# Kernel tuning notes

Hardware: AMD Instinct MI355X
Metric: run time of the kernel (lower is better)

The kernel has to match this reference:

```python
import jax, jax.numpy as jnp
import numpy as np

N_NODES = 20000
N_EDGES = 320000
D_IN = 32 * 32 * 3  # 3072


def gcn_layer(x, W, b, src, dst):
    # Lign GCN(nn.Linear): dense transform, then sum-aggregation over edges
    h = x @ W + b                                            # [N, d_out]
    msg = jax.ops.segment_sum(h[src], dst, num_segments=N_NODES)  # neighbor sum
    return h + msg                                           # self + neighbors


def setup_inputs() -> dict:
    key = jax.random.key(0)
    ks = jax.random.split(key, 12)
    def w(k, shape, fan_in):
        return jax.random.normal(k, shape, jnp.float32) * (1.0 / np.sqrt(fan_in))
    return {
        "features": jax.random.normal(ks[0], (N_NODES, D_IN), jnp.float32),
        "src": jax.random.randint(ks[1], (N_EDGES,), 0, N_NODES),
        "dst": jax.random.randint(ks[2], (N_EDGES,), 0, N_NODES),
        "W1": w(ks[3], (D_IN, 1000), D_IN), "b1": jnp.zeros((1000,), jnp.float32),
        "W2": w(ks[4], (1000, 300), 1000), "b2": jnp.zeros((300,), jnp.float32),
        "W3": w(ks[5], (300, 20), 300),    "b3": jnp.zeros((20,), jnp.float32),
        "W4": w(ks[6], (20, 10), 20),      "b4": jnp.zeros((10,), jnp.float32),
    }


def reference(features, src, dst, W1, b1, W2, b2, W3, b3, W4, b4):
    x = features.reshape(-1, D_IN)
    x = jax.nn.relu(gcn_layer(x, W1, b1, src, dst))
    x = jax.nn.relu(gcn_layer(x, W2, b2, src, dst))
    x = gcn_layer(x, W3, b3, src, dst)
    return jnp.tanh(gcn_layer(x, W4, b4, src, dst))
```

## Files before the change

kernel.cpp:

```cpp
#include <hip/hip_runtime.h>
#include <math.h>

#define N_NODES 20000
#define N_EDGES 320000
#define D_IN    3072

#define M_PAD   20096
#define N1_PAD  1024
#define LDH1    1024
#define K2_PAD  1024
#define N2_PAD  384
#define LDH2    384

typedef short bf16x8 __attribute__((ext_vector_type(8)));
typedef float f32x4  __attribute__((ext_vector_type(4)));
typedef int   i32x4  __attribute__((ext_vector_type(4)));

#define GLOAD_LDS16(g, l) __builtin_amdgcn_global_load_lds( \
    (const __attribute__((address_space(1))) void*)(g),     \
    (__attribute__((address_space(3))) void*)(l), 16, 0, 0)

__device__ inline unsigned short f2bf(float x) {
    union { float f; unsigned u; } v; v.f = x;
    unsigned r = (v.u + 0x7FFFu + ((v.u >> 16) & 1u)) >> 16;
    return (unsigned short)r;
}
__device__ inline float bf2f(unsigned short h) {
    union { float f; unsigned u; } v; v.u = ((unsigned)h) << 16;
    return v.f;
}


__global__ void zero_counts_kernel(int* __restrict__ counts) {
    int i = blockIdx.x * blockDim.x + threadIdx.x;
    if (i < N_NODES) counts[i] = 0;
}

__global__ void count_kernel(const int* __restrict__ dst, int* __restrict__ counts) {
    int e = blockIdx.x * blockDim.x + threadIdx.x;
    if (e < N_EDGES) atomicAdd(&counts[dst[e]], 1);
}

__global__ void scan_kernel(const int* __restrict__ counts, int* __restrict__ row_start,
                            int* __restrict__ cursor) {
    __shared__ int part[1024];
    const int T = 1024;
    int t = threadIdx.x;
    const int chunk = (N_NODES + T - 1) / T;
    int lo = t * chunk;
    int hi = lo + chunk; if (hi > N_NODES) hi = N_NODES;
    int s = 0;
    for (int i = lo; i < hi; ++i) s += counts[i];
    part[t] = s;
    __syncthreads();
    for (int off = 1; off < T; off <<= 1) {
        int v = (t >= off) ? part[t - off] : 0;
        __syncthreads();
        part[t] += v;
        __syncthreads();
    }
    int run = part[t] - s;
    for (int i = lo; i < hi; ++i) {
        row_start[i] = run;
        cursor[i] = run;
        run += counts[i];
    }
    if (t == T - 1) row_start[N_NODES] = run;
}

__global__ void scatter_kernel(const int* __restrict__ src, const int* __restrict__ dst,
                               int* __restrict__ cursor, int* __restrict__ esrc) {
    int e = blockIdx.x * blockDim.x + threadIdx.x;
    if (e < N_EDGES) {
        int pos = atomicAdd(&cursor[dst[e]], 1);
        esrc[pos] = src[e];
    }
}


__global__ __launch_bounds__(256)
void convA_i8_kernel(const float* __restrict__ X, signed char* __restrict__ Aq1,
                     signed char* __restrict__ Aq2, float* __restrict__ sA) {
    __shared__ float red[256];
    const int row = blockIdx.x;
    const int t = threadIdx.x;
    const float* xr = X + (size_t)row * D_IN;
    float v[12];
    float mx = 0.f;
    #pragma unroll
    for (int c = 0; c < 3; ++c) {
        float4 f = *reinterpret_cast<const float4*>(&xr[(t + c * 256) * 4]);
        v[c*4+0] = f.x; v[c*4+1] = f.y; v[c*4+2] = f.z; v[c*4+3] = f.w;
        mx = fmaxf(mx, fmaxf(fmaxf(fabsf(f.x), fabsf(f.y)), fmaxf(fabsf(f.z), fabsf(f.w))));
    }
    red[t] = mx;
    __syncthreads();
    for (int off = 128; off > 0; off >>= 1) {
        if (t < off) red[t] = fmaxf(red[t], red[t + off]);
        __syncthreads();
    }
    const float rmax = red[0];
    const float s   = (rmax > 0.f) ? rmax / 16256.f : 1.f;
    const float inv = 16256.f / ((rmax > 0.f) ? rmax : 1.f);
    if (t == 0) sA[row] = s;
    #pragma unroll
    for (int c = 0; c < 3; ++c) {
        signed char q1v[4], q2v[4];
        #pragma unroll
        for (int e = 0; e < 4; ++e) {
            int q = __float2int_rn(v[c*4+e] * inv);
            q = min(max(q, -16256), 16256);
            int q1 = (q + 64) >> 7;
            int q2 = q - (q1 << 7);
            q1v[e] = (signed char)q1; q2v[e] = (signed char)q2;
        }
        size_t base = (size_t)row * D_IN + (size_t)(t + c * 256) * 4;
        *reinterpret_cast<char4*>(&Aq1[base]) = make_char4(q1v[0], q1v[1], q1v[2], q1v[3]);
        *reinterpret_cast<char4*>(&Aq2[base]) = make_char4(q2v[0], q2v[1], q2v[2], q2v[3]);
    }
}


__global__ __launch_bounds__(256)
void zero_swbits_kernel(unsigned* __restrict__ bits, int NPAD) {
    int n = blockIdx.x * blockDim.x + threadIdx.x;
    if (n < NPAD) bits[n] = 0u;
}

__global__ __launch_bounds__(256)
void colmaxW_kernel(const float* __restrict__ W, unsigned* __restrict__ bits,
                    int K, int N, int KCHUNK) {
    int n = blockIdx.x * blockDim.x + threadIdx.x;
    if (n >= N) return;
    int k0 = blockIdx.y * KCHUNK;
    int k1 = min(k0 + KCHUNK, K);
    float mx = 0.f;
    for (int k = k0; k < k1; ++k)
        mx = fmaxf(mx, fabsf(W[(size_t)k * N + n]));
    atomicMax(&bits[n], __float_as_uint(mx));
}

__global__ __launch_bounds__(256)
void finalize_sw_kernel(unsigned* __restrict__ bits, float* __restrict__ sW, int NPAD) {
    int n = blockIdx.x * blockDim.x + threadIdx.x;
    if (n >= NPAD) return;
    float mx = __uint_as_float(bits[n]);
    sW[n] = (mx > 0.f) ? mx / 16256.f : 1.f;
}

__global__ __launch_bounds__(256)
void convW_i8_kernel(const float* __restrict__ W, const float* __restrict__ sW,
                     signed char* __restrict__ Wq1T, signed char* __restrict__ Wq2T,
                     int K, int N, int K_PAD) {
    __shared__ float sh[32][33];
    const int t  = threadIdx.x;
    const int tx = t & 31;
    const int ty = t >> 5;
    const int n0 = blockIdx.x * 32;
    const int k0 = blockIdx.y * 32;
    #pragma unroll
    for (int it = 0; it < 4; ++it) {
        int k = k0 + ty + it * 8;
        int n = n0 + tx;
        sh[ty + it * 8][tx] = (k < K && n < N) ? W[(size_t)k * N + n] : 0.f;
    }
    __syncthreads();
    #pragma unroll
    for (int it = 0; it < 4; ++it) {
        int n = n0 + ty + it * 8;
        int k = k0 + tx;
        float v = sh[tx][ty + it * 8];
        float s = sW[n];
        int q = __float2int_rn(v / s);
        q = min(max(q, -16256), 16256);
        int q1 = (q + 64) >> 7;
        int q2 = q - (q1 << 7);
        Wq1T[(size_t)n * K_PAD + k] = (signed char)q1;
        Wq2T[(size_t)n * K_PAD + k] = (signed char)q2;
    }
}


#define GBM 128
#define GBN 128

#define ISSUE2I(p0, p1, ss) do { \
    GLOAD_LDS16(p0, &lds[ss][wid * 1024]); \
    GLOAD_LDS16(p1, &lds[ss][wid * 1024 + 4096]); \
    p0 += 64; p1 += 64; } while (0)

__global__ __launch_bounds__(256, 2)
void gemm_i8_mfma_kernel(const signed char* __restrict__ Aq1,
                         const signed char* __restrict__ Aq2,
                         const signed char* __restrict__ Bq1T,
                         const signed char* __restrict__ Bq2T,
                         const float* __restrict__ sA, const float* __restrict__ sB,
                         const float* __restrict__ bias, float* __restrict__ H,
                         int K, int NB, int ldh, int nbias) {
    __shared__ __align__(16) char lds[4][8192];

    const int t    = threadIdx.x;
    const int wid  = t >> 6;
    const int lane = t & 63;
    const int wr   = wid >> 1;
    const int wc   = wid & 1;

    const int orig = blockIdx.x;
    const int nwg  = gridDim.x;
    const int xcd  = orig & 7, loc = orig >> 3;
    const int q    = nwg >> 3, r = nwg & 7;
    const int wgid = (xcd < r ? xcd * (q + 1) : r * (q + 1) + (xcd - r) * q) + loc;
    const int m0   = (wgid / NB) * GBM;
    const int n0   = (wgid % NB) * GBN;

    i32x4 accH[4][4] = {};
    i32x4 accM[4][4] = {};

    const int byt0 = wid * 1024 + lane * 16;
    const int byt1 = byt0 + 4096;
    const int r0 = byt0 >> 6, r1 = byt1 >> 6;
    const int cs0 = (byt0 & 63) ^ (((r0 >> 1) & 3) << 4);
    const int cs1 = (byt1 & 63) ^ (((r1 >> 1) & 3) << 4);

    const signed char* pA10 = Aq1  + (size_t)(m0 + r0) * K + cs0;
    const signed char* pA11 = Aq1  + (size_t)(m0 + r1) * K + cs1;
    const signed char* pA20 = Aq2  + (size_t)(m0 + r0) * K + cs0;
    const signed char* pA21 = Aq2  + (size_t)(m0 + r1) * K + cs1;
    const signed char* pB10 = Bq1T + (size_t)(n0 + r0) * K + cs0;
    const signed char* pB11 = Bq1T + (size_t)(n0 + r1) * K + cs1;
    const signed char* pB20 = Bq2T + (size_t)(n0 + r0) * K + cs0;
    const signed char* pB21 = Bq2T + (size_t)(n0 + r1) * K + cs1;

    const int fr   = lane & 15;
    const int kbs  = ((lane >> 4) << 4) ^ (((fr >> 1) & 3) << 4);
    const int arow = wr * 64;
    const int brow = wc * 64;

    ISSUE2I(pA10, pA11, 0);
    ISSUE2I(pB10, pB11, 2);
    ISSUE2I(pB20, pB21, 3);
    ISSUE2I(pA20, pA21, 1);

    const int NT = K >> 6;
    i32x4 a1[4], b1[4], b2[4], a2[4];

    for (int tt = 0; tt < NT; ++tt) {
        if (tt == 0) asm volatile("s_waitcnt vmcnt(4)" ::: "memory");
        else         asm volatile("s_waitcnt vmcnt(2)" ::: "memory");
        __builtin_amdgcn_s_barrier();
        #pragma unroll
        for (int i = 0; i < 4; ++i)
            a1[i] = *(const i32x4*)(&lds[0][(arow + i * 16 + fr) * 64 + kbs]);
        #pragma unroll
        for (int j = 0; j < 4; ++j)
            b1[j] = *(const i32x4*)(&lds[2][(brow + j * 16 + fr) * 64 + kbs]);
        if (tt > 0) ISSUE2I(pA20, pA21, 1);
        __builtin_amdgcn_s_setprio(1);
        #pragma unroll
        for (int i = 0; i < 4; ++i)
            #pragma unroll
            for (int j = 0; j < 4; ++j)
                accH[i][j] = __builtin_amdgcn_mfma_i32_16x16x64_i8(a1[i], b1[j], accH[i][j], 0, 0, 0);
        __builtin_amdgcn_s_setprio(0);
        asm volatile("s_waitcnt vmcnt(2)" ::: "memory");
        __builtin_amdgcn_s_barrier();
        #pragma unroll
        for (int j = 0; j < 4; ++j)
            b2[j] = *(const i32x4*)(&lds[3][(brow + j * 16 + fr) * 64 + kbs]);
        if (tt < NT - 1) {
            ISSUE2I(pA10, pA11, 0);
            ISSUE2I(pB10, pB11, 2);
        }
        __builtin_amdgcn_s_setprio(1);
        #pragma unroll
        for (int i = 0; i < 4; ++i)
            #pragma unroll
            for (int j = 0; j < 4; ++j)
                accM[i][j] = __builtin_amdgcn_mfma_i32_16x16x64_i8(a1[i], b2[j], accM[i][j], 0, 0, 0);
        __builtin_amdgcn_s_setprio(0);
        if (tt < NT - 1) asm volatile("s_waitcnt vmcnt(4)" ::: "memory");
        else             asm volatile("s_waitcnt vmcnt(0)" ::: "memory");
        __builtin_amdgcn_s_barrier();
        #pragma unroll
        for (int i = 0; i < 4; ++i)
            a2[i] = *(const i32x4*)(&lds[1][(arow + i * 16 + fr) * 64 + kbs]);
        if (tt < NT - 1) ISSUE2I(pB20, pB21, 3);
        __builtin_amdgcn_s_setprio(1);
        #pragma unroll
        for (int i = 0; i < 4; ++i)
            #pragma unroll
            for (int j = 0; j < 4; ++j)
                accM[i][j] = __builtin_amdgcn_mfma_i32_16x16x64_i8(a2[i], b1[j], accM[i][j], 0, 0, 0);
        __builtin_amdgcn_s_setprio(0);
    }

    #pragma unroll
    for (int i = 0; i < 4; ++i) {
        #pragma unroll
        for (int j = 0; j < 4; ++j) {
            int row = m0 + wr * 64 + i * 16 + (lane >> 4) * 4;
            int col = n0 + wc * 64 + j * 16 + (lane & 15);
            float bv = (col < nbias) ? bias[col] : 0.f;
            float sw = sB[col];
            #pragma unroll
            for (int r2 = 0; r2 < 4; ++r2) {
                float sa = sA[row + r2];
                float v = sa * sw * (16384.f * (float)accH[i][j][r2] + 128.f * (float)accM[i][j][r2]) + bv;
                H[(size_t)(row + r2) * ldh + col] = v;
            }
        }
    }
}


__global__ __launch_bounds__(256)
void convW_kernel(const float* __restrict__ W, unsigned short* __restrict__ WhiT,
                  unsigned short* __restrict__ WloT, int K, int N, int K_PAD) {
    __shared__ float sh[32][33];
    const int t  = threadIdx.x;
    const int tx = t & 31;
    const int ty = t >> 5;
    const int n0 = blockIdx.x * 32;
    const int k0 = blockIdx.y * 32;
    #pragma unroll
    for (int it = 0; it < 4; ++it) {
        int k = k0 + ty + it * 8;
        int n = n0 + tx;
        sh[ty + it * 8][tx] = (k < K && n < N) ? W[(size_t)k * N + n] : 0.f;
    }
    __syncthreads();
    #pragma unroll
    for (int it = 0; it < 4; ++it) {
        int n = n0 + ty + it * 8;
        int k = k0 + tx;
        float v = sh[tx][ty + it * 8];
        unsigned short h = f2bf(v);
        unsigned short l = f2bf(v - bf2f(h));
        WhiT[(size_t)n * K_PAD + k] = h;
        WloT[(size_t)n * K_PAD + k] = l;
    }
}


#define GBK 32

#define ISSUE2(p0, p1, ss) do { \
    GLOAD_LDS16(p0, &lds[ss][wid * 1024]); \
    GLOAD_LDS16(p1, &lds[ss][wid * 1024 + 4096]); \
    p0 += GBK; p1 += GBK; } while (0)

__global__ __launch_bounds__(256, 3)
void gemm_split_mfma_kernel(const unsigned short* __restrict__ Ahi,
                            const unsigned short* __restrict__ Alo,
                            const unsigned short* __restrict__ BhiT,
                            const unsigned short* __restrict__ BloT,
                            const float* __restrict__ bias, float* __restrict__ H,
                            int K, int NB, int ldh, int nbias) {
    __shared__ __align__(16) char lds[4][8192];

    const int t    = threadIdx.x;
    const int wid  = t >> 6;
    const int lane = t & 63;
    const int wr   = wid >> 1;
    const int wc   = wid & 1;

    const int orig = blockIdx.x;
    const int nwg  = gridDim.x;
    const int xcd  = orig & 7, loc = orig >> 3;
    const int q    = nwg >> 3, r = nwg & 7;
    const int wgid = (xcd < r ? xcd * (q + 1) : r * (q + 1) + (xcd - r) * q) + loc;
    const int m0   = (wgid / NB) * GBM;
    const int n0   = (wgid % NB) * GBN;

    f32x4 acc[4][4] = {};

    const int byt0 = wid * 1024 + lane * 16;
    const int byt1 = byt0 + 4096;
    const int r0 = byt0 >> 6, r1 = byt1 >> 6;
    const int cs0 = (byt0 & 63) ^ (((r0 >> 1) & 3) << 4);
    const int cs1 = (byt1 & 63) ^ (((r1 >> 1) & 3) << 4);

    const unsigned short* pAh0 = Ahi  + (size_t)(m0 + r0) * K + (cs0 >> 1);
    const unsigned short* pAh1 = Ahi  + (size_t)(m0 + r1) * K + (cs1 >> 1);
    const unsigned short* pAl0 = Alo  + (size_t)(m0 + r0) * K + (cs0 >> 1);
    const unsigned short* pAl1 = Alo  + (size_t)(m0 + r1) * K + (cs1 >> 1);
    const unsigned short* pBh0 = BhiT + (size_t)(n0 + r0) * K + (cs0 >> 1);
    const unsigned short* pBh1 = BhiT + (size_t)(n0 + r1) * K + (cs1 >> 1);
    const unsigned short* pBl0 = BloT + (size_t)(n0 + r0) * K + (cs0 >> 1);
    const unsigned short* pBl1 = BloT + (size_t)(n0 + r1) * K + (cs1 >> 1);

    const int fr   = lane & 15;
    const int kbs  = ((lane >> 4) << 4) ^ (((fr >> 1) & 3) << 4);
    const int arow = wr * 64;
    const int brow = wc * 64;

    ISSUE2(pAh0, pAh1, 0);
    ISSUE2(pBh0, pBh1, 2);
    ISSUE2(pBl0, pBl1, 3);
    ISSUE2(pAl0, pAl1, 1);

    const int NT = K >> 5;
    bf16x8 ahi[4], bhi[4], blo[4], alo[4];

    for (int tt = 0; tt < NT; ++tt) {
        if (tt == 0) asm volatile("s_waitcnt vmcnt(4)" ::: "memory");
        else         asm volatile("s_waitcnt vmcnt(2)" ::: "memory");
        __builtin_amdgcn_s_barrier();
        #pragma unroll
        for (int i = 0; i < 4; ++i)
            ahi[i] = *(const bf16x8*)(&lds[0][(arow + i * 16 + fr) * 64 + kbs]);
        #pragma unroll
        for (int j = 0; j < 4; ++j)
            bhi[j] = *(const bf16x8*)(&lds[2][(brow + j * 16 + fr) * 64 + kbs]);
        if (tt > 0) ISSUE2(pAl0, pAl1, 1);
        __builtin_amdgcn_s_setprio(1);
        #pragma unroll
        for (int i = 0; i < 4; ++i)
            #pragma unroll
            for (int j = 0; j < 4; ++j)
                acc[i][j] = __builtin_amdgcn_mfma_f32_16x16x32_bf16(ahi[i], bhi[j], acc[i][j], 0, 0, 0);
        __builtin_amdgcn_s_setprio(0);
        asm volatile("s_waitcnt vmcnt(2)" ::: "memory");
        __builtin_amdgcn_s_barrier();
        #pragma unroll
        for (int j = 0; j < 4; ++j)
            blo[j] = *(const bf16x8*)(&lds[3][(brow + j * 16 + fr) * 64 + kbs]);
        if (tt < NT - 1) {
            ISSUE2(pAh0, pAh1, 0);
            ISSUE2(pBh0, pBh1, 2);
        }
        __builtin_amdgcn_s_setprio(1);
        #pragma unroll
        for (int i = 0; i < 4; ++i)
            #pragma unroll
            for (int j = 0; j < 4; ++j)
                acc[i][j] = __builtin_amdgcn_mfma_f32_16x16x32_bf16(ahi[i], blo[j], acc[i][j], 0, 0, 0);
        __builtin_amdgcn_s_setprio(0);
        if (tt < NT - 1) asm volatile("s_waitcnt vmcnt(4)" ::: "memory");
        else             asm volatile("s_waitcnt vmcnt(0)" ::: "memory");
        __builtin_amdgcn_s_barrier();
        #pragma unroll
        for (int i = 0; i < 4; ++i)
            alo[i] = *(const bf16x8*)(&lds[1][(arow + i * 16 + fr) * 64 + kbs]);
        if (tt < NT - 1) ISSUE2(pBl0, pBl1, 3);
        __builtin_amdgcn_s_setprio(1);
        #pragma unroll
        for (int i = 0; i < 4; ++i)
            #pragma unroll
            for (int j = 0; j < 4; ++j)
                acc[i][j] = __builtin_amdgcn_mfma_f32_16x16x32_bf16(alo[i], bhi[j], acc[i][j], 0, 0, 0);
        __builtin_amdgcn_s_setprio(0);
    }

    #pragma unroll
    for (int i = 0; i < 4; ++i) {
        #pragma unroll
        for (int j = 0; j < 4; ++j) {
            int row = m0 + wr * 64 + i * 16 + (lane >> 4) * 4;
            int col = n0 + wc * 64 + j * 16 + (lane & 15);
            float bv = (col < nbias) ? bias[col] : 0.f;
            #pragma unroll
            for (int r2 = 0; r2 < 4; ++r2)
                H[(size_t)(row + r2) * ldh + col] = acc[i][j][r2] + bv;
        }
    }
}


#define BM 64
#define BN 64
#define BKT 16
#define TM 4
#define TN 4

__global__ __launch_bounds__(256)
void gemm_bias_kernel(const float* __restrict__ X, const float* __restrict__ W,
                      const float* __restrict__ bias, float* __restrict__ H,
                      int M, int N, int K) {
    __shared__ float As[BKT][BM];
    __shared__ float Bs[BKT][BN];

    const int t  = threadIdx.x;
    const int tx = t & 15;
    const int ty = t >> 4;
    const int m0 = blockIdx.y * BM;
    const int n0 = blockIdx.x * BN;

    float acc[TM][TN] = {};

    const int arow = t >> 2;
    const int ak0  = (t & 3) * 4;
    const int brow = t >> 4;
    const int bn0  = (t & 15) * 4;

    for (int k0 = 0; k0 < K; k0 += BKT) {
        {
            float4 v = make_float4(0.f, 0.f, 0.f, 0.f);
            int gm = m0 + arow;
            int gk = k0 + ak0;
            if (gm < M) {
                if (gk + 3 < K) {
                    v = *reinterpret_cast<const float4*>(&X[(long)gm * K + gk]);
                } else {
                    float tmp[4] = {0.f, 0.f, 0.f, 0.f};
                    for (int i = 0; i < 4; ++i)
                        if (gk + i < K) tmp[i] = X[(long)gm * K + gk + i];
                    v = make_float4(tmp[0], tmp[1], tmp[2], tmp[3]);
                }
            }
            As[ak0 + 0][arow] = v.x;
            As[ak0 + 1][arow] = v.y;
            As[ak0 + 2][arow] = v.z;
            As[ak0 + 3][arow] = v.w;
        }
        {
            float4 v = make_float4(0.f, 0.f, 0.f, 0.f);
            int gk = k0 + brow;
            int gn = n0 + bn0;
            if (gk < K) {
                if (gn + 3 < N) {
                    v = *reinterpret_cast<const float4*>(&W[(long)gk * N + gn]);
                } else {
                    float tmp[4] = {0.f, 0.f, 0.f, 0.f};
                    for (int i = 0; i < 4; ++i)
                        if (gn + i < N) tmp[i] = W[(long)gk * N + gn + i];
                    v = make_float4(tmp[0], tmp[1], tmp[2], tmp[3]);
                }
            }
            *reinterpret_cast<float4*>(&Bs[brow][bn0]) = v;
        }
        __syncthreads();

        #pragma unroll
        for (int kk = 0; kk < BKT; ++kk) {
            float a[TM], b[TN];
            *reinterpret_cast<float4*>(a) = *reinterpret_cast<const float4*>(&As[kk][ty * TM]);
            *reinterpret_cast<float4*>(b) = *reinterpret_cast<const float4*>(&Bs[kk][tx * TN]);
            #pragma unroll
            for (int i = 0; i < TM; ++i)
                #pragma unroll
                for (int j = 0; j < TN; ++j)
                    acc[i][j] += a[i] * b[j];
        }
        __syncthreads();
    }

    #pragma unroll
    for (int i = 0; i < TM; ++i) {
        int gm = m0 + ty * TM + i;
        if (gm >= M) continue;
        #pragma unroll
        for (int j = 0; j < TN; ++j) {
            int gn = n0 + tx * TN + j;
            if (gn < N) H[(long)gm * N + gn] = acc[i][j] + bias[gn];
        }
    }
}


__global__ __launch_bounds__(256)
void aggregate_bf16_kernel(const float* __restrict__ H, const int* __restrict__ row_start,
                           const int* __restrict__ esrc, unsigned short* __restrict__ Xhi,
                           unsigned short* __restrict__ Xlo, int d, int ld_in, int kpad) {
    const int node = blockIdx.x;
    const int f = threadIdx.x * 4;
    if (f >= kpad) return;
    if (f >= d) {
        ushort4 z = make_ushort4(0, 0, 0, 0);
        *reinterpret_cast<ushort4*>(&Xhi[(size_t)node * kpad + f]) = z;
        *reinterpret_cast<ushort4*>(&Xlo[(size_t)node * kpad + f]) = z;
        return;
    }
    const int beg = row_start[node];
    const int end = row_start[node + 1];
    float4 acc = *reinterpret_cast<const float4*>(&H[(size_t)node * ld_in + f]);
    for (int i = beg; i < end; ++i) {
        float4 v = *reinterpret_cast<const float4*>(&H[(size_t)esrc[i] * ld_in + f]);
        acc.x += v.x; acc.y += v.y; acc.z += v.z; acc.w += v.w;
    }
    acc.x = fmaxf(acc.x, 0.f); acc.y = fmaxf(acc.y, 0.f);
    acc.z = fmaxf(acc.z, 0.f); acc.w = fmaxf(acc.w, 0.f);
    unsigned short h0 = f2bf(acc.x), h1 = f2bf(acc.y), h2 = f2bf(acc.z), h3 = f2bf(acc.w);
    unsigned short l0 = f2bf(acc.x - bf2f(h0));
    unsigned short l1 = f2bf(acc.y - bf2f(h1));
    unsigned short l2 = f2bf(acc.z - bf2f(h2));
    unsigned short l3 = f2bf(acc.w - bf2f(h3));
    *reinterpret_cast<ushort4*>(&Xhi[(size_t)node * kpad + f]) = make_ushort4(h0, h1, h2, h3);
    *reinterpret_cast<ushort4*>(&Xlo[(size_t)node * kpad + f]) = make_ushort4(l0, l1, l2, l3);
}

__global__ __launch_bounds__(128)
void agg2_gemm3_kernel(const float* __restrict__ H2, const int* __restrict__ row_start,
                       const int* __restrict__ esrc, const float* __restrict__ W3,
                       const float* __restrict__ b3, float* __restrict__ h3) {
    __shared__ float x3s[304];
    __shared__ float part[6][20];
    const int node = blockIdx.x;
    const int t = threadIdx.x;
    const int beg = row_start[node];
    const int end = row_start[node + 1];
    if (t < 75) {
        const int f = t * 4;
        float4 acc = *reinterpret_cast<const float4*>(&H2[(size_t)node * LDH2 + f]);
        for (int i = beg; i < end; ++i) {
            float4 v = *reinterpret_cast<const float4*>(&H2[(size_t)esrc[i] * LDH2 + f]);
            acc.x += v.x; acc.y += v.y; acc.z += v.z; acc.w += v.w;
        }
        x3s[f + 0] = fmaxf(acc.x, 0.f);
        x3s[f + 1] = fmaxf(acc.y, 0.f);
        x3s[f + 2] = fmaxf(acc.z, 0.f);
        x3s[f + 3] = fmaxf(acc.w, 0.f);
    }
    __syncthreads();
    if (t < 120) {
        const int j = t % 20, g = t / 20;
        float s = 0.f;
        #pragma unroll 5
        for (int k = g * 50; k < g * 50 + 50; ++k)
            s += x3s[k] * W3[k * 20 + j];
        part[g][j] = s;
    }
    __syncthreads();
    if (t < 20) {
        float s = b3[t];
        #pragma unroll
        for (int g = 0; g < 6; ++g) s += part[g][t];
        h3[(size_t)node * 20 + t] = s;
    }
}

__global__ __launch_bounds__(64)
void agg3_gemm4_kernel(const float* __restrict__ h3, const int* __restrict__ row_start,
                       const int* __restrict__ esrc, const float* __restrict__ W4,
                       const float* __restrict__ b4, float* __restrict__ h4) {
    __shared__ float x4s[20];
    const int node = blockIdx.x;
    const int t = threadIdx.x;
    const int beg = row_start[node];
    const int end = row_start[node + 1];
    if (t < 20) {
        float acc = h3[(size_t)node * 20 + t];
        for (int i = beg; i < end; ++i)
            acc += h3[(size_t)esrc[i] * 20 + t];
        x4s[t] = acc;
    }
    __syncthreads();
    if (t < 10) {
        float s = b4[t];
        #pragma unroll
        for (int k = 0; k < 20; ++k) s += x4s[k] * W4[k * 10 + t];
        h4[(size_t)node * 10 + t] = s;
    }
}

template <int ACT>
__global__ __launch_bounds__(64)
void aggregate_small_kernel(const float* __restrict__ H, const int* __restrict__ row_start,
                            const int* __restrict__ esrc, float* __restrict__ out,
                            int d, int ld_in, int ld_out) {
    const int node = blockIdx.x;
    const int f = threadIdx.x;
    if (f >= d) return;
    const int beg = row_start[node];
    const int end = row_start[node + 1];
    float acc = H[(size_t)node * ld_in + f];
    for (int i = beg; i < end; ++i)
        acc += H[(size_t)esrc[i] * ld_in + f];
    if (ACT == 1) acc = fmaxf(acc, 0.f);
    if (ACT == 2) acc = tanhf(acc);
    out[(size_t)node * ld_out + f] = acc;
}

template <int ACT>
__global__ __launch_bounds__(256)
void aggregate_kernel(const float* __restrict__ H, const int* __restrict__ row_start,
                      const int* __restrict__ esrc, float* __restrict__ out,
                      int d, int ld_in) {
    const int node = blockIdx.x;
    const int t = threadIdx.x;
    const int beg = row_start[node];
    const int end = row_start[node + 1];
    float acc[4] = {0.f, 0.f, 0.f, 0.f};
    #pragma unroll
    for (int j = 0; j < 4; ++j) {
        int f = t + j * 256;
        if (f < d) acc[j] = H[(size_t)node * ld_in + f];
    }
    for (int i = beg; i < end; ++i) {
        const size_t b = (size_t)esrc[i] * ld_in;
        #pragma unroll
        for (int j = 0; j < 4; ++j) {
            int f = t + j * 256;
            if (f < d) acc[j] += H[b + f];
        }
    }
    #pragma unroll
    for (int j = 0; j < 4; ++j) {
        int f = t + j * 256;
        if (f < d) {
            float v = acc[j];
            if (ACT == 1) v = fmaxf(v, 0.f);
            if (ACT == 2) v = tanhf(v);
            out[(size_t)node * d + f] = v;
        }
    }
}


extern "C" void kernel_launch(void* const* d_in, const int* in_sizes, int n_in,
                              void* d_out, int out_size, void* d_ws, size_t ws_size,
                              hipStream_t stream) {
    const float* features = (const float*)d_in[0];
    const int*   src      = (const int*)d_in[1];
    const int*   dst      = (const int*)d_in[2];
    const float* W1 = (const float*)d_in[3];  const float* b1 = (const float*)d_in[4];
    const float* W2 = (const float*)d_in[5];  const float* b2 = (const float*)d_in[6];
    const float* W3 = (const float*)d_in[7];  const float* b3 = (const float*)d_in[8];
    const float* W4 = (const float*)d_in[9];  const float* b4 = (const float*)d_in[10];
    float* out = (float*)d_out;
    char* ws = (char*)d_ws;

    const size_t SZ_AQ   = (size_t)M_PAD * D_IN;
    const size_t OFF_AQ1 = 0;
    const size_t OFF_AQ2 = SZ_AQ;
    const size_t OFF_H1  = 2 * SZ_AQ;
    const size_t SZ_H1   = (size_t)M_PAD * LDH1 * 4;
    const size_t OFF_W1Q1 = OFF_H1 + SZ_H1;
    const size_t SZ_W1Q  = (size_t)N1_PAD * D_IN;
    const size_t OFF_W1Q2 = OFF_W1Q1 + SZ_W1Q;
    const size_t OFF_SA  = OFF_W1Q2 + SZ_W1Q;
    const size_t OFF_SW1 = OFF_SA + (size_t)M_PAD * 4;
    const size_t OFF_W2T = OFF_SW1 + (size_t)N1_PAD * 4;
    const size_t SZ_W2T  = (size_t)N2_PAD * K2_PAD * 2;
    const size_t OFF_CSR = OFF_W2T + 2 * SZ_W2T;
    const size_t SZ_CSR  = (size_t)(N_NODES * 3 + 1 + N_EDGES) * 4;
    const size_t WS_NEED = OFF_CSR + SZ_CSR;

    const size_t OFF_X2H = 0;
    const size_t OFF_X2L = (size_t)M_PAD * K2_PAD * 2;
    const size_t OFF_H2  = 2 * OFF_X2L;
    const size_t OFF_H3  = OFF_H1;
    const size_t OFF_H4  = OFF_H1 + 1600000;

    const bool use_mfma = (ws_size >= WS_NEED);
    size_t csr_off = use_mfma ? OFF_CSR : (size_t)2 * N_NODES * 1000 * 4;
    int* counts    = (int*)(ws + csr_off);
    int* row_start = counts + N_NODES;
    int* cursor    = row_start + N_NODES + 1;
    int* esrc      = cursor + N_NODES;

    zero_counts_kernel<<<(N_NODES + 255) / 256, 256, 0, stream>>>(counts);
    count_kernel<<<(N_EDGES + 255) / 256, 256, 0, stream>>>(dst, counts);
    scan_kernel<<<1, 1024, 0, stream>>>(counts, row_start, cursor);
    scatter_kernel<<<(N_EDGES + 255) / 256, 256, 0, stream>>>(src, dst, cursor, esrc);

    if (use_mfma) {
        signed char*    Aq1   = (signed char*)(ws + OFF_AQ1);
        signed char*    Aq2   = (signed char*)(ws + OFF_AQ2);
        float*          H1    = (float*)(ws + OFF_H1);
        signed char*    W1q1T = (signed char*)(ws + OFF_W1Q1);
        signed char*    W1q2T = (signed char*)(ws + OFF_W1Q2);
        float*          sA    = (float*)(ws + OFF_SA);
        float*          sW1   = (float*)(ws + OFF_SW1);
        unsigned*       sW1b  = (unsigned*)(ws + OFF_SW1);
        unsigned short* W2hiT = (unsigned short*)(ws + OFF_W2T);
        unsigned short* W2loT = (unsigned short*)(ws + OFF_W2T + SZ_W2T);
        unsigned short* X2hi  = (unsigned short*)(ws + OFF_X2H);
        unsigned short* X2lo  = (unsigned short*)(ws + OFF_X2L);
        float*          H2    = (float*)(ws + OFF_H2);
        float*          h3    = (float*)(ws + OFF_H3);
        float*          h4    = (float*)(ws + OFF_H4);

        convA_i8_kernel<<<N_NODES, 256, 0, stream>>>(features, Aq1, Aq2, sA);
        zero_swbits_kernel<<<N1_PAD / 256, 256, 0, stream>>>(sW1b, N1_PAD);
        colmaxW_kernel<<<dim3((1000 + 255) / 256, 24), 256, 0, stream>>>(W1, sW1b, D_IN, 1000, 128);
        finalize_sw_kernel<<<N1_PAD / 256, 256, 0, stream>>>(sW1b, sW1, N1_PAD);
        convW_i8_kernel<<<dim3(N1_PAD / 32, D_IN / 32), 256, 0, stream>>>(
            W1, sW1, W1q1T, W1q2T, D_IN, 1000, D_IN);
        gemm_i8_mfma_kernel<<<(N1_PAD / GBN) * (M_PAD / GBM), 256, 0, stream>>>(
            Aq1, Aq2, W1q1T, W1q2T, sA, sW1, b1, H1, D_IN, N1_PAD / GBN, LDH1, 1000);
        aggregate_bf16_kernel<<<N_NODES, 256, 0, stream>>>(
            H1, row_start, esrc, X2hi, X2lo, 1000, LDH1, K2_PAD);

        convW_kernel<<<dim3(N2_PAD / 32, K2_PAD / 32), 256, 0, stream>>>(W2, W2hiT, W2loT, 1000, 300, K2_PAD);
        gemm_split_mfma_kernel<<<(N2_PAD / GBN) * (M_PAD / GBM), 256, 0, stream>>>(
            X2hi, X2lo, W2hiT, W2loT, b2, H2, K2_PAD, N2_PAD / GBN, LDH2, 300);

        agg2_gemm3_kernel<<<N_NODES, 128, 0, stream>>>(H2, row_start, esrc, W3, b3, h3);
        agg3_gemm4_kernel<<<N_NODES, 64, 0, stream>>>(h3, row_start, esrc, W4, b4, h4);
        aggregate_small_kernel<2><<<N_NODES, 64, 0, stream>>>(h4, row_start, esrc, out, 10, 10, 10);
    } else {
        const size_t BUF = (size_t)N_NODES * 1000 * 4;
        float* bufA = (float*)ws;
        float* bufB = (float*)(ws + BUF);

        dim3 g1((1000 + BN - 1) / BN, (N_NODES + BM - 1) / BM);
        gemm_bias_kernel<<<g1, 256, 0, stream>>>(features, W1, b1, bufA, N_NODES, 1000, D_IN);
        aggregate_kernel<1><<<N_NODES, 256, 0, stream>>>(bufA, row_start, esrc, bufB, 1000, 1000);

        dim3 g2((300 + BN - 1) / BN, (N_NODES + BM - 1) / BM);
        gemm_bias_kernel<<<g2, 256, 0, stream>>>(bufB, W2, b2, bufA, N_NODES, 300, 1000);
        aggregate_kernel<1><<<N_NODES, 256, 0, stream>>>(bufA, row_start, esrc, bufB, 300, 300);

        dim3 g3((20 + BN - 1) / BN, (N_NODES + BM - 1) / BM);
        gemm_bias_kernel<<<g3, 256, 0, stream>>>(bufB, W3, b3, bufA, N_NODES, 20, 300);
        aggregate_kernel<0><<<N_NODES, 256, 0, stream>>>(bufA, row_start, esrc, bufB, 20, 20);

        dim3 g4((10 + BN - 1) / BN, (N_NODES + BM - 1) / BM);
        gemm_bias_kernel<<<g4, 256, 0, stream>>>(bufB, W4, b4, bufA, N_NODES, 10, 20);
        aggregate_kernel<2><<<N_NODES, 256, 0, stream>>>(bufA, row_start, esrc, out, 10, 10);
    }
}
```

Baseline: 727.4 us.

## Store layer-1 output as bf16 and run layer-2 GEMM with split int8 MFMA

The layer-1 GEMM is templated so it can write its output as bf16 instead of fp32, which halves the bytes the first aggregation gathers. The aggregation now quantizes each aggregated node row into two int8 parts with a per-row scale. The layer-2 GEMM reuses the split int8 MFMA kernel in place of the bf16 hi/lo split kernel, with W2 quantized the same way. Launch bounds are raised to 3 waves per SIMD. The risks are lower precision from storing H1 as bf16 and from per-row int8 quantization, a block-wide max reduction added to the aggregation, and possible register pressure at the higher occupancy.

Result: slower. 1.418 ms (+95.0%).

```diff
diff --git a/kernel.cpp b/kernel.cpp
--- a/kernel.cpp
+++ b/kernel.cpp
@@ -189,13 +189,14 @@
     GLOAD_LDS16(p1, &lds[ss][wid * 1024 + 4096]); \
     p0 += 64; p1 += 64; } while (0)
 
-__global__ __launch_bounds__(256, 2)
+template <int OUTBF>
+__global__ __launch_bounds__(256, 3)
 void gemm_i8_mfma_kernel(const signed char* __restrict__ Aq1,
                          const signed char* __restrict__ Aq2,
                          const signed char* __restrict__ Bq1T,
                          const signed char* __restrict__ Bq2T,
                          const float* __restrict__ sA, const float* __restrict__ sB,
-                         const float* __restrict__ bias, float* __restrict__ H,
+                         const float* __restrict__ bias, void* __restrict__ Hout,
                          int K, int NB, int ldh, int nbias) {
     __shared__ __align__(16) char lds[4][8192];
 
@@ -306,162 +307,9 @@
             for (int r2 = 0; r2 < 4; ++r2) {
                 float sa = sA[row + r2];
                 float v = sa * sw * (16384.f * (float)accH[i][j][r2] + 128.f * (float)accM[i][j][r2]) + bv;
-                H[(size_t)(row + r2) * ldh + col] = v;
+                if (OUTBF) ((unsigned short*)Hout)[(size_t)(row + r2) * ldh + col] = f2bf(v);
+                else       ((float*)Hout)[(size_t)(row + r2) * ldh + col] = v;
             }
-        }
-    }
-}
-
-
-__global__ __launch_bounds__(256)
-void convW_kernel(const float* __restrict__ W, unsigned short* __restrict__ WhiT,
-                  unsigned short* __restrict__ WloT, int K, int N, int K_PAD) {
-    __shared__ float sh[32][33];
-    const int t  = threadIdx.x;
-    const int tx = t & 31;
-    const int ty = t >> 5;
-    const int n0 = blockIdx.x * 32;
-    const int k0 = blockIdx.y * 32;
-    #pragma unroll
-    for (int it = 0; it < 4; ++it) {
-        int k = k0 + ty + it * 8;
-        int n = n0 + tx;
-        sh[ty + it * 8][tx] = (k < K && n < N) ? W[(size_t)k * N + n] : 0.f;
-    }
-    __syncthreads();
-    #pragma unroll
-    for (int it = 0; it < 4; ++it) {
-        int n = n0 + ty + it * 8;
-        int k = k0 + tx;
-        float v = sh[tx][ty + it * 8];
-        unsigned short h = f2bf(v);
-        unsigned short l = f2bf(v - bf2f(h));
-        WhiT[(size_t)n * K_PAD + k] = h;
-        WloT[(size_t)n * K_PAD + k] = l;
-    }
-}
-
-
-#define GBK 32
-
-#define ISSUE2(p0, p1, ss) do { \
-    GLOAD_LDS16(p0, &lds[ss][wid * 1024]); \
-    GLOAD_LDS16(p1, &lds[ss][wid * 1024 + 4096]); \
-    p0 += GBK; p1 += GBK; } while (0)
-
-__global__ __launch_bounds__(256, 3)
-void gemm_split_mfma_kernel(const unsigned short* __restrict__ Ahi,
-                            const unsigned short* __restrict__ Alo,
-                            const unsigned short* __restrict__ BhiT,
-                            const unsigned short* __restrict__ BloT,
-                            const float* __restrict__ bias, float* __restrict__ H,
-                            int K, int NB, int ldh, int nbias) {
-    __shared__ __align__(16) char lds[4][8192];
-
-    const int t    = threadIdx.x;
-    const int wid  = t >> 6;
-    const int lane = t & 63;
-    const int wr   = wid >> 1;
-    const int wc   = wid & 1;
-
-    const int orig = blockIdx.x;
-    const int nwg  = gridDim.x;
-    const int xcd  = orig & 7, loc = orig >> 3;
-    const int q    = nwg >> 3, r = nwg & 7;
-    const int wgid = (xcd < r ? xcd * (q + 1) : r * (q + 1) + (xcd - r) * q) + loc;
-    const int m0   = (wgid / NB) * GBM;
-    const int n0   = (wgid % NB) * GBN;
-
-    f32x4 acc[4][4] = {};
-
-    const int byt0 = wid * 1024 + lane * 16;
-    const int byt1 = byt0 + 4096;
-    const int r0 = byt0 >> 6, r1 = byt1 >> 6;
-    const int cs0 = (byt0 & 63) ^ (((r0 >> 1) & 3) << 4);
-    const int cs1 = (byt1 & 63) ^ (((r1 >> 1) & 3) << 4);
-
-    const unsigned short* pAh0 = Ahi  + (size_t)(m0 + r0) * K + (cs0 >> 1);
-    const unsigned short* pAh1 = Ahi  + (size_t)(m0 + r1) * K + (cs1 >> 1);
-    const unsigned short* pAl0 = Alo  + (size_t)(m0 + r0) * K + (cs0 >> 1);
-    const unsigned short* pAl1 = Alo  + (size_t)(m0 + r1) * K + (cs1 >> 1);
-    const unsigned short* pBh0 = BhiT + (size_t)(n0 + r0) * K + (cs0 >> 1);
-    const unsigned short* pBh1 = BhiT + (size_t)(n0 + r1) * K + (cs1 >> 1);
-    const unsigned short* pBl0 = BloT + (size_t)(n0 + r0) * K + (cs0 >> 1);
-    const unsigned short* pBl1 = BloT + (size_t)(n0 + r1) * K + (cs1 >> 1);
-
-    const int fr   = lane & 15;
-    const int kbs  = ((lane >> 4) << 4) ^ (((fr >> 1) & 3) << 4);
-    const int arow = wr * 64;
-    const int brow = wc * 64;
-
-    ISSUE2(pAh0, pAh1, 0);
-    ISSUE2(pBh0, pBh1, 2);
-    ISSUE2(pBl0, pBl1, 3);
-    ISSUE2(pAl0, pAl1, 1);
-
-    const int NT = K >> 5;
-    bf16x8 ahi[4], bhi[4], blo[4], alo[4];
-
-    for (int tt = 0; tt < NT; ++tt) {
-        if (tt == 0) asm volatile("s_waitcnt vmcnt(4)" ::: "memory");
-        else         asm volatile("s_waitcnt vmcnt(2)" ::: "memory");
-        __builtin_amdgcn_s_barrier();
-        #pragma unroll
-        for (int i = 0; i < 4; ++i)
-            ahi[i] = *(const bf16x8*)(&lds[0][(arow + i * 16 + fr) * 64 + kbs]);
-        #pragma unroll
-        for (int j = 0; j < 4; ++j)
-            bhi[j] = *(const bf16x8*)(&lds[2][(brow + j * 16 + fr) * 64 + kbs]);
-        if (tt > 0) ISSUE2(pAl0, pAl1, 1);
-        __builtin_amdgcn_s_setprio(1);
-        #pragma unroll
-        for (int i = 0; i < 4; ++i)
-            #pragma unroll
-            for (int j = 0; j < 4; ++j)
-                acc[i][j] = __builtin_amdgcn_mfma_f32_16x16x32_bf16(ahi[i], bhi[j], acc[i][j], 0, 0, 0);
-        __builtin_amdgcn_s_setprio(0);
-        asm volatile("s_waitcnt vmcnt(2)" ::: "memory");
-        __builtin_amdgcn_s_barrier();
-        #pragma unroll
-        for (int j = 0; j < 4; ++j)
-            blo[j] = *(const bf16x8*)(&lds[3][(brow + j * 16 + fr) * 64 + kbs]);
-        if (tt < NT - 1) {
-            ISSUE2(pAh0, pAh1, 0);
-            ISSUE2(pBh0, pBh1, 2);
-        }
-        __builtin_amdgcn_s_setprio(1);
-        #pragma unroll
-        for (int i = 0; i < 4; ++i)
-            #pragma unroll
-            for (int j = 0; j < 4; ++j)
-                acc[i][j] = __builtin_amdgcn_mfma_f32_16x16x32_bf16(ahi[i], blo[j], acc[i][j], 0, 0, 0);
-        __builtin_amdgcn_s_setprio(0);
-        if (tt < NT - 1) asm volatile("s_waitcnt vmcnt(4)" ::: "memory");
-        else             asm volatile("s_waitcnt vmcnt(0)" ::: "memory");
-        __builtin_amdgcn_s_barrier();
-        #pragma unroll
-        for (int i = 0; i < 4; ++i)
-            alo[i] = *(const bf16x8*)(&lds[1][(arow + i * 16 + fr) * 64 + kbs]);
-        if (tt < NT - 1) ISSUE2(pBl0, pBl1, 3);
-        __builtin_amdgcn_s_setprio(1);
-        #pragma unroll
-        for (int i = 0; i < 4; ++i)
-            #pragma unroll
-            for (int j = 0; j < 4; ++j)
-                acc[i][j] = __builtin_amdgcn_mfma_f32_16x16x32_bf16(alo[i], bhi[j], acc[i][j], 0, 0, 0);
-        __builtin_amdgcn_s_setprio(0);
-    }
-
-    #pragma unroll
-    for (int i = 0; i < 4; ++i) {
-        #pragma unroll
-        for (int j = 0; j < 4; ++j) {
-            int row = m0 + wr * 64 + i * 16 + (lane >> 4) * 4;
-            int col = n0 + wc * 64 + j * 16 + (lane & 15);
-            float bv = (col < nbias) ? bias[col] : 0.f;
-            #pragma unroll
-            for (int r2 = 0; r2 < 4; ++r2)
-                H[(size_t)(row + r2) * ldh + col] = acc[i][j][r2] + bv;
         }
     }
 }
@@ -559,34 +407,52 @@
 
 
 __global__ __launch_bounds__(256)
-void aggregate_bf16_kernel(const float* __restrict__ H, const int* __restrict__ row_start,
-                           const int* __restrict__ esrc, unsigned short* __restrict__ Xhi,
-                           unsigned short* __restrict__ Xlo, int d, int ld_in, int kpad) {
+void aggregate_i8_kernel(const unsigned short* __restrict__ H1,
+                         const int* __restrict__ row_start, const int* __restrict__ esrc,
+                         signed char* __restrict__ Xq1, signed char* __restrict__ Xq2,
+                         float* __restrict__ sX, int d, int ld_in, int kpad) {
+    __shared__ float red[256];
     const int node = blockIdx.x;
-    const int f = threadIdx.x * 4;
-    if (f >= kpad) return;
-    if (f >= d) {
-        ushort4 z = make_ushort4(0, 0, 0, 0);
-        *reinterpret_cast<ushort4*>(&Xhi[(size_t)node * kpad + f]) = z;
-        *reinterpret_cast<ushort4*>(&Xlo[(size_t)node * kpad + f]) = z;
-        return;
-    }
+    const int t = threadIdx.x;
+    const int f = t * 4;
     const int beg = row_start[node];
     const int end = row_start[node + 1];
-    float4 acc = *reinterpret_cast<const float4*>(&H[(size_t)node * ld_in + f]);
-    for (int i = beg; i < end; ++i) {
-        float4 v = *reinterpret_cast<const float4*>(&H[(size_t)esrc[i] * ld_in + f]);
-        acc.x += v.x; acc.y += v.y; acc.z += v.z; acc.w += v.w;
-    }
-    acc.x = fmaxf(acc.x, 0.f); acc.y = fmaxf(acc.y, 0.f);
-    acc.z = fmaxf(acc.z, 0.f); acc.w = fmaxf(acc.w, 0.f);
-    unsigned short h0 = f2bf(acc.x), h1 = f2bf(acc.y), h2 = f2bf(acc.z), h3 = f2bf(acc.w);
-    unsigned short l0 = f2bf(acc.x - bf2f(h0));
-    unsigned short l1 = f2bf(acc.y - bf2f(h1));
-    unsigned short l2 = f2bf(acc.z - bf2f(h2));
-    unsigned short l3 = f2bf(acc.w - bf2f(h3));
-    *reinterpret_cast<ushort4*>(&Xhi[(size_t)node * kpad + f]) = make_ushort4(h0, h1, h2, h3);
-    *reinterpret_cast<ushort4*>(&Xlo[(size_t)node * kpad + f]) = make_ushort4(l0, l1, l2, l3);
+
+    float a[4] = {0.f, 0.f, 0.f, 0.f};
+    if (f < d) {
+        ushort4 v = *reinterpret_cast<const ushort4*>(&H1[(size_t)node * ld_in + f]);
+        a[0] = bf2f(v.x); a[1] = bf2f(v.y); a[2] = bf2f(v.z); a[3] = bf2f(v.w);
+        for (int i = beg; i < end; ++i) {
+            ushort4 w = *reinterpret_cast<const ushort4*>(&H1[(size_t)esrc[i] * ld_in + f]);
+            a[0] += bf2f(w.x); a[1] += bf2f(w.y); a[2] += bf2f(w.z); a[3] += bf2f(w.w);
+        }
+        a[0] = fmaxf(a[0], 0.f); a[1] = fmaxf(a[1], 0.f);
+        a[2] = fmaxf(a[2], 0.f); a[3] = fmaxf(a[3], 0.f);
+    }
+    float mx = fmaxf(fmaxf(a[0], a[1]), fmaxf(a[2], a[3]));
+    red[t] = mx;
+    __syncthreads();
+    for (int off = 128; off > 0; off >>= 1) {
+        if (t < off) red[t] = fmaxf(red[t], red[t + off]);
+        __syncthreads();
+    }
+    const float rmax = red[0];
+    const float s   = (rmax > 0.f) ? rmax / 16256.f : 1.f;
+    const float inv = 16256.f / ((rmax > 0.f) ? rmax : 1.f);
+    if (t == 0) sX[node] = s;
+    if (f < kpad) {
+        signed char q1v[4], q2v[4];
+        #pragma unroll
+        for (int e = 0; e < 4; ++e) {
+            int q = (f < d) ? __float2int_rn(a[e] * inv) : 0;
+            q = min(max(q, 0), 16256);
+            int q1 = (q + 64) >> 7;
+            int q2 = q - (q1 << 7);
+            q1v[e] = (signed char)q1; q2v[e] = (signed char)q2;
+        }
+        *reinterpret_cast<char4*>(&Xq1[(size_t)node * kpad + f]) = make_char4(q1v[0], q1v[1], q1v[2], q1v[3]);
+        *reinterpret_cast<char4*>(&Xq2[(size_t)node * kpad + f]) = make_char4(q2v[0], q2v[1], q2v[2], q2v[3]);
+    }
 }
 
 __global__ __launch_bounds__(128)
@@ -720,27 +586,32 @@
     float* out = (float*)d_out;
     char* ws = (char*)d_ws;
 
-    const size_t SZ_AQ   = (size_t)M_PAD * D_IN;
-    const size_t OFF_AQ1 = 0;
-    const size_t OFF_AQ2 = SZ_AQ;
-    const size_t OFF_H1  = 2 * SZ_AQ;
-    const size_t SZ_H1   = (size_t)M_PAD * LDH1 * 4;
+    const size_t SZ_AQ    = (size_t)M_PAD * D_IN;
+    const size_t OFF_AQ1  = 0;
+    const size_t OFF_AQ2  = SZ_AQ;
+    const size_t OFF_H1   = 2 * SZ_AQ;
+    const size_t SZ_H1    = (size_t)M_PAD * LDH1 * 2;
     const size_t OFF_W1Q1 = OFF_H1 + SZ_H1;
-    const size_t SZ_W1Q  = (size_t)N1_PAD * D_IN;
+    const size_t SZ_W1Q   = (size_t)N1_PAD * D_IN;
     const size_t OFF_W1Q2 = OFF_W1Q1 + SZ_W1Q;
-    const size_t OFF_SA  = OFF_W1Q2 + SZ_W1Q;
-    const size_t OFF_SW1 = OFF_SA + (size_t)M_PAD * 4;
-    const size_t OFF_W2T = OFF_SW1 + (size_t)N1_PAD * 4;
-    const size_t SZ_W2T  = (size_t)N2_PAD * K2_PAD * 2;
-    const size_t OFF_CSR = OFF_W2T + 2 * SZ_W2T;
-    const size_t SZ_CSR  = (size_t)(N_NODES * 3 + 1 + N_EDGES) * 4;
-    const size_t WS_NEED = OFF_CSR + SZ_CSR;
-
-    const size_t OFF_X2H = 0;
-    const size_t OFF_X2L = (size_t)M_PAD * K2_PAD * 2;
-    const size_t OFF_H2  = 2 * OFF_X2L;
-    const size_t OFF_H3  = OFF_H1;
-    const size_t OFF_H4  = OFF_H1 + 1600000;
+    const size_t OFF_SA   = OFF_W1Q2 + SZ_W1Q;
+    const size_t SZ_SA    = (size_t)M_PAD * 4;
+    const size_t OFF_SW1  = OFF_SA + SZ_SA;
+    const size_t OFF_W2Q1 = OFF_SW1 + 4096;
+    const size_t SZ_W2Q   = (size_t)N2_PAD * K2_PAD;
+    const size_t OFF_W2Q2 = OFF_W2Q1 + SZ_W2Q;
+    const size_t OFF_SW2  = OFF_W2Q2 + SZ_W2Q;
+    const size_t OFF_SA2  = OFF_SW2 + 4096;
+    const size_t OFF_CSR  = OFF_SA2 + SZ_SA;
+    const size_t SZ_CSR   = (size_t)(N_NODES * 3 + 1 + N_EDGES) * 4;
+    const size_t WS_NEED  = OFF_CSR + SZ_CSR;
+
+    const size_t OFF_X2Q1 = 0;
+    const size_t SZ_X2Q   = (size_t)M_PAD * K2_PAD;
+    const size_t OFF_X2Q2 = SZ_X2Q;
+    const size_t OFF_H2   = 2 * SZ_X2Q;
+    const size_t OFF_H3   = OFF_H1;
+    const size_t OFF_H4   = OFF_H1 + 1600000;
 
     const bool use_mfma = (ws_size >= WS_NEED);
     size_t csr_off = use_mfma ? OFF_CSR : (size_t)2 * N_NODES * 1000 * 4;
@@ -757,16 +628,19 @@
     if (use_mfma) {
         signed char*    Aq1   = (signed char*)(ws + OFF_AQ1);
         signed char*    Aq2   = (signed char*)(ws + OFF_AQ2);
-        float*          H1    = (float*)(ws + OFF_H1);
+        unsigned short* H1    = (unsigned short*)(ws + OFF_H1);
         signed char*    W1q1T = (signed char*)(ws + OFF_W1Q1);
         signed char*    W1q2T = (signed char*)(ws + OFF_W1Q2);
         float*          sA    = (float*)(ws + OFF_SA);
         float*          sW1   = (float*)(ws + OFF_SW1);
         unsigned*       sW1b  = (unsigned*)(ws + OFF_SW1);
-        unsigned short* W2hiT = (unsigned short*)(ws + OFF_W2T);
-        unsigned short* W2loT = (unsigned short*)(ws + OFF_W2T + SZ_W2T);
-        unsigned short* X2hi  = (unsigned short*)(ws + OFF_X2H);
-        unsigned short* X2lo  = (unsigned short*)(ws + OFF_X2L);
+        signed char*    W2q1T = (signed char*)(ws + OFF_W2Q1);
+        signed char*    W2q2T = (signed char*)(ws + OFF_W2Q2);
+        float*          sW2   = (float*)(ws + OFF_SW2);
+        unsigned*       sW2b  = (unsigned*)(ws + OFF_SW2);
+        signed char*    X2q1  = (signed char*)(ws + OFF_X2Q1);
+        signed char*    X2q2  = (signed char*)(ws + OFF_X2Q2);
+        float*          sA2   = (float*)(ws + OFF_SA2);
         float*          H2    = (float*)(ws + OFF_H2);
         float*          h3    = (float*)(ws + OFF_H3);
         float*          h4    = (float*)(ws + OFF_H4);
@@ -777,14 +651,18 @@
         finalize_sw_kernel<<<N1_PAD / 256, 256, 0, stream>>>(sW1b, sW1, N1_PAD);
         convW_i8_kernel<<<dim3(N1_PAD / 32, D_IN / 32), 256, 0, stream>>>(
             W1, sW1, W1q1T, W1q2T, D_IN, 1000, D_IN);
-        gemm_i8_mfma_kernel<<<(N1_PAD / GBN) * (M_PAD / GBM), 256, 0, stream>>>(
+        gemm_i8_mfma_kernel<1><<<(N1_PAD / GBN) * (M_PAD / GBM), 256, 0, stream>>>(
             Aq1, Aq2, W1q1T, W1q2T, sA, sW1, b1, H1, D_IN, N1_PAD / GBN, LDH1, 1000);
-        aggregate_bf16_kernel<<<N_NODES, 256, 0, stream>>>(
-            H1, row_start, esrc, X2hi, X2lo, 1000, LDH1, K2_PAD);
-
-        convW_kernel<<<dim3(N2_PAD / 32, K2_PAD / 32), 256, 0, stream>>>(W2, W2hiT, W2loT, 1000, 300, K2_PAD);
-        gemm_split_mfma_kernel<<<(N2_PAD / GBN) * (M_PAD / GBM), 256, 0, stream>>>(
-            X2hi, X2lo, W2hiT, W2loT, b2, H2, K2_PAD, N2_PAD / GBN, LDH2, 300);
+        aggregate_i8_kernel<<<N_NODES, 256, 0, stream>>>(
+            H1, row_start, esrc, X2q1, X2q2, sA2, 1000, LDH1, K2_PAD);
+
+        zero_swbits_kernel<<<(N2_PAD + 255) / 256, 256, 0, stream>>>(sW2b, N2_PAD);
+        colmaxW_kernel<<<dim3((300 + 255) / 256, 8), 256, 0, stream>>>(W2, sW2b, 1000, 300, 128);
+        finalize_sw_kernel<<<(N2_PAD + 255) / 256, 256, 0, stream>>>(sW2b, sW2, N2_PAD);
+        convW_i8_kernel<<<dim3(N2_PAD / 32, K2_PAD / 32), 256, 0, stream>>>(
+            W2, sW2, W2q1T, W2q2T, 1000, 300, K2_PAD);
+        gemm_i8_mfma_kernel<0><<<(N2_PAD / GBN) * (M_PAD / GBM), 256, 0, stream>>>(
+            X2q1, X2q2, W2q1T, W2q2T, sA2, sW2, b2, H2, K2_PAD, N2_PAD / GBN, LDH2, 300);
 
         agg2_gemm3_kernel<<<N_NODES, 128, 0, stream>>>(H2, row_start, esrc, W3, b3, h3);
         agg3_gemm4_kernel<<<N_NODES, 64, 0, stream>>>(h3, row_start, esrc, W4, b4, h4);
```
